# Kernel optimization log

Measured on AMD Instinct MI355X. Metric: run time of the kernel, lower is better.

## Reference

```python
import jax, jax.numpy as jnp
import numpy as np

B, FP, SP = 256, 80, 160          # graphs, features/graph, sentences/graph
H, NH = 128, 4                    # hidden size, attention heads
DH = H // NH
NPG = FP + SP + 2                 # nodes per graph (features, sents, user, item)
N = B * NPG                       # total nodes = 61952
E = 1_000_000


def setup_inputs() -> dict:
    key = jax.random.key(0)
    ks = jax.random.split(key, 24)
    s = 0.05  # small init like the module's uniform(-0.001,0.001) spirit, but non-degenerate
    inp = {
        "fid": jax.random.randint(ks[0], (B * FP,), 0, 10000, dtype=jnp.int32),
        "sid": jax.random.randint(ks[1], (B * SP,), 0, 500000, dtype=jnp.int32),
        "uid": jax.random.randint(ks[2], (B,), 0, 100000, dtype=jnp.int32),
        "iid": jax.random.randint(ks[3], (B,), 0, 50000, dtype=jnp.int32),
        "edge_src": jax.random.randint(ks[4], (E,), 0, N, dtype=jnp.int32),
        "edge_dst": jax.random.randint(ks[5], (E,), 0, N, dtype=jnp.int32),
        "user_tab": jax.random.normal(ks[6], (100000, H), jnp.float32),
        "item_tab": jax.random.normal(ks[7], (50000, H), jnp.float32),
        "feat_tab": jax.random.normal(ks[8], (10000, H), jnp.float32),
        "sent_tab": jax.random.normal(ks[9], (500000, H), jnp.float32),
        "W_feat": jax.random.normal(ks[10], (H, H), jnp.float32) * s,
        "W_sent": jax.random.normal(ks[11], (H, H), jnp.float32) * s,
        "W_user": jax.random.normal(ks[12], (H, H), jnp.float32) * s,
        "W_item": jax.random.normal(ks[13], (H, H), jnp.float32) * s,
        "W_gat": jax.random.normal(ks[14], (H, H), jnp.float32) * s,
        "attn_l": jax.random.normal(ks[15], (NH, DH), jnp.float32) * s,
        "attn_r": jax.random.normal(ks[16], (NH, DH), jnp.float32) * s,
        "w_sent_out": jax.random.normal(ks[17], (H, 1), jnp.float32) * s,
        "b_sent_out": jnp.zeros((1,), jnp.float32),
        "w_feat_out": jax.random.normal(ks[18], (H, 1), jnp.float32) * s,
        "b_feat_out": jnp.zeros((1,), jnp.float32),
    }
    return inp


def _forward(fid, sid, uid, iid, edge_src, edge_dst,
             user_tab, item_tab, feat_tab, sent_tab,
             W_feat, W_sent, W_user, W_item,
             W_gat, attn_l, attn_r,
             w_sent_out, b_sent_out, w_feat_out, b_feat_out):
    # --- embed + bias-free projection for each node type ---
    f_node = feat_tab[fid] @ W_feat          # [B*FP, H]
    s_node = sent_tab[sid] @ W_sent          # [B*SP, H]
    u_node = user_tab[uid] @ W_user          # [B, H]
    i_node = item_tab[iid] @ W_item          # [B, H]

    # --- per-graph node layout: [features | sentences | user | item] ---
    x = jnp.concatenate([
        f_node.reshape(B, FP, H),
        s_node.reshape(B, SP, H),
        u_node[:, None, :],
        i_node[:, None, :],
    ], axis=1).reshape(N, H)                 # [N, H]

    # --- single-layer multi-head GAT over edge list ---
    z = (x @ W_gat).reshape(N, NH, DH)       # [N, NH, DH]
    el = jnp.sum(z * attn_l, axis=-1)        # [N, NH]
    er = jnp.sum(z * attn_r, axis=-1)        # [N, NH]
    e = jax.nn.leaky_relu(el[edge_src] + er[edge_dst], 0.2)  # [E, NH]
    m = jax.ops.segment_max(e, edge_dst, num_segments=N)     # per-dst max
    ex = jnp.exp(e - m[edge_dst])
    den = jax.ops.segment_sum(ex, edge_dst, num_segments=N)
    alpha = ex / (den[edge_dst] + 1e-9)                      # edge softmax [E, NH]
    agg = jax.ops.segment_sum(alpha[:, :, None] * z[edge_src], edge_dst,
                              num_segments=N)                # [N, NH, DH]
    h = jax.nn.elu(agg.reshape(N, H))                        # [N, H]

    # --- gather sentence / feature node states and score ---
    base = jnp.arange(B)[:, None] * NPG
    f_idx = (base + jnp.arange(FP)[None, :]).reshape(-1)      # [B*FP]
    s_idx = (base + FP + jnp.arange(SP)[None, :]).reshape(-1)  # [B*SP]
    sent_scores = (h[s_idx] @ w_sent_out + b_sent_out)[:, 0]  # [B*SP]
    feat_scores = (h[f_idx] @ w_feat_out + b_feat_out)[:, 0]  # [B*FP]
    return jnp.concatenate([sent_scores, feat_scores])        # [B*(SP+FP)]


def reference(fid, sid, uid, iid, edge_src, edge_dst,
              user_tab, item_tab, feat_tab, sent_tab,
              W_feat, W_sent, W_user, W_item,
              W_gat, attn_l, attn_r,
              w_sent_out, b_sent_out, w_feat_out, b_feat_out):
    return _forward(fid, sid, uid, iid, edge_src, edge_dst,
                    user_tab, item_tab, feat_tab, sent_tab,
                    W_feat, W_sent, W_user, W_item,
                    W_gat, attn_l, attn_r,
                    w_sent_out, b_sent_out, w_feat_out, b_feat_out)
```

## Files before the change

kernel.cpp:

```cpp
#include <hip/hip_runtime.h>
#include <cmath>

#define BB  256
#define FPN 80
#define SPN 160
#define NPGc 242
#define NNc (BB*NPGc)
#define NBKT 242
#define CAPSH 13
#define BCAP (1<<CAPSH)
#define NPART 512

typedef __attribute__((ext_vector_type(8))) short bf16x8;
typedef __attribute__((ext_vector_type(4))) float f32x4;

static __device__ __forceinline__ unsigned short f2bf(float f) {
    unsigned u = __float_as_uint(f);
    unsigned r = (u + 0x7fffu + ((u >> 16) & 1u)) >> 16;
    return (unsigned short)r;
}
static __device__ __forceinline__ float bf2f(unsigned short u) {
    return __uint_as_float(((unsigned)u) << 16);
}
static __device__ __forceinline__ unsigned pk2(float a, float b) {
    return (unsigned)f2bf(a) | ((unsigned)f2bf(b) << 16);
}

__global__ __launch_bounds__(256) void k_wc(
    const float* __restrict__ Wf, const float* __restrict__ Ws,
    const float* __restrict__ Wu, const float* __restrict__ Wi,
    const float* __restrict__ Wg, unsigned short* __restrict__ WcT,
    int* __restrict__ bucket_cur)
{
    int b = blockIdx.x;
    int t = threadIdx.x;
    if (b >= 64) {
        if (t < NBKT) bucket_cur[t * 16] = t << CAPSH;
        return;
    }
    int type = b >> 4;
    int rowbase = (b & 15) * 8;
    const float* Wt = type == 0 ? Wf : type == 1 ? Ws : type == 2 ? Wu : Wi;
    int j = t & 127;
    int half = t >> 7;
    for (int i = rowbase + half; i < rowbase + 8; i += 2) {
        float acc = 0.f;
        for (int k = 0; k < 128; ++k)
            acc = fmaf(Wt[i * 128 + k], Wg[k * 128 + j], acc);
        WcT[type * 16384 + j * 128 + i] = f2bf(acc);
    }
}

__global__ __launch_bounds__(256) void k_part(
    const int* __restrict__ esrc, const int* __restrict__ edst, int E,
    int* __restrict__ bucket_cur, unsigned* __restrict__ bucketed)
{
    __shared__ int h[NBKT];
    __shared__ int base_[NBKT];
    int b = blockIdx.x, t = threadIdx.x;
    for (int j = t; j < NBKT; j += 256) h[j] = 0;
    __syncthreads();
    int CH = (E + NPART - 1) / NPART;
    int start = b * CH, lim = min(start + CH, E);
    for (int i = start + t; i < lim; i += 256)
        atomicAdd(&h[edst[i] >> 8], 1);
    __syncthreads();
    for (int j = t; j < NBKT; j += 256) {
        int c = h[j];
        base_[j] = c ? atomicAdd(&bucket_cur[j * 16], c) : 0;
        h[j] = 0;
    }
    __syncthreads();
    for (int i = start + t; i < lim; i += 256) {
        int d = edst[i];
        int bk = d >> 8;
        int pos = base_[bk] + atomicAdd(&h[bk], 1);
        bucketed[pos] = ((unsigned)(d & 255) << 16) | (unsigned)esrc[i];
    }
}

struct SortSh { int h[256]; unsigned short s16[BCAP]; };
struct EmbSh  { unsigned short sWt[128 * 128], sE[32 * 128], sZ[32 * 128]; };
union  ShU    { SortSh sort; EmbSh emb; };

__global__ __launch_bounds__(256) void k_fused(
    const int* __restrict__ bucket_cur, const unsigned* __restrict__ bucketed,
    unsigned short* __restrict__ srcs16, int* __restrict__ off, int* __restrict__ cnt,
    const int* __restrict__ fid, const int* __restrict__ sid,
    const int* __restrict__ uid, const int* __restrict__ iid,
    const float* __restrict__ feat_tab, const float* __restrict__ sent_tab,
    const float* __restrict__ user_tab, const float* __restrict__ item_tab,
    const unsigned short* __restrict__ WcT, const float* __restrict__ attn_l,
    const float* __restrict__ attn_r,
    unsigned short* __restrict__ zb, float* __restrict__ el, float* __restrict__ er)
{
    __shared__ ShU sh;
    int b = blockIdx.x, t = threadIdx.x;

    if (b < NBKT) {
        int bk = b;
        int beg = bk << CAPSH;
        int m = bucket_cur[bk * 16] - beg;
        int* h = sh.sort.h;
        h[t] = 0;
        __syncthreads();
        for (int i = t; i < m; i += 256)
            atomicAdd(&h[(bucketed[beg + i] >> 16) & 255], 1);
        __syncthreads();
        int myc = h[t];
        for (int d = 1; d < 256; d <<= 1) {
            int add = (t >= d) ? h[t - d] : 0;
            __syncthreads();
            h[t] += add;
            __syncthreads();
        }
        int node = (bk << 8) + t;
        off[node] = beg + h[t] - myc;
        cnt[node] = myc;
        __syncthreads();
        for (int i = t; i < m; i += 256) {
            unsigned u = bucketed[beg + i];
            int low = (u >> 16) & 255;
            int pos = atomicSub(&h[low], 1) - 1;
            sh.sort.s16[pos] = (unsigned short)(u & 0xFFFFu);
        }
        __syncthreads();
        for (int i = t; i < m; i += 256) srcs16[beg + i] = sh.sort.s16[i];
        return;
    }

    int eb = b - NBKT;
    int type, q0;
    if (eb < 640)       { type = 0; q0 = eb * 32; }
    else if (eb < 1920) { type = 1; q0 = (eb - 640) * 32; }
    else if (eb < 1928) { type = 2; q0 = (eb - 1920) * 32; }
    else                { type = 3; q0 = (eb - 1928) * 32; }

    {
        const uint4* src = (const uint4*)(WcT + type * 16384);
        uint4* dst = (uint4*)sh.emb.sWt;
#pragma unroll
        for (int i = 0; i < 8; ++i) dst[t + i * 256] = src[t + i * 256];
    }

    int row = t >> 3, part = t & 7;
    int q = q0 + row;
    int id; const float* tab;
    if (type == 0)      { id = fid[q]; tab = feat_tab; }
    else if (type == 1) { id = sid[q]; tab = sent_tab; }
    else if (type == 2) { id = uid[q]; tab = user_tab; }
    else                { id = iid[q]; tab = item_tab; }
    {
        const float4* gsrc = (const float4*)(tab + (long long)id * 128) + part * 4;
        float4 v0 = gsrc[0], v1 = gsrc[1], v2 = gsrc[2], v3 = gsrc[3];
        uint4 p0 = {pk2(v0.x, v0.y), pk2(v0.z, v0.w), pk2(v1.x, v1.y), pk2(v1.z, v1.w)};
        uint4 p1 = {pk2(v2.x, v2.y), pk2(v2.z, v2.w), pk2(v3.x, v3.y), pk2(v3.z, v3.w)};
        uint4* se = (uint4*)&sh.emb.sE[row * 128 + part * 16];
        se[0] = p0; se[1] = p1;
    }
    __syncthreads();

    {
        int lane = t & 63, w = t >> 6;
        int l15 = lane & 15, l4 = lane >> 4;
        int cb = w * 32;
        f32x4 acc00 = {0, 0, 0, 0}, acc01 = {0, 0, 0, 0};
        f32x4 acc10 = {0, 0, 0, 0}, acc11 = {0, 0, 0, 0};
        const unsigned short* sE = sh.emb.sE;
        const unsigned short* sWt = sh.emb.sWt;
#pragma unroll
        for (int kb = 0; kb < 4; ++kb) {
            int ko = kb * 32 + l4 * 8;
            bf16x8 a0 = *(const bf16x8*)&sE[l15 * 128 + ko];
            bf16x8 a1 = *(const bf16x8*)&sE[(l15 + 16) * 128 + ko];
            bf16x8 b0 = *(const bf16x8*)&sWt[(cb + l15) * 128 + ko];
            bf16x8 b1 = *(const bf16x8*)&sWt[(cb + 16 + l15) * 128 + ko];
            acc00 = __builtin_amdgcn_mfma_f32_16x16x32_bf16(a0, b0, acc00, 0, 0, 0);
            acc01 = __builtin_amdgcn_mfma_f32_16x16x32_bf16(a0, b1, acc01, 0, 0, 0);
            acc10 = __builtin_amdgcn_mfma_f32_16x16x32_bf16(a1, b0, acc10, 0, 0, 0);
            acc11 = __builtin_amdgcn_mfma_f32_16x16x32_bf16(a1, b1, acc11, 0, 0, 0);
        }
        unsigned short* sZ = sh.emb.sZ;
#pragma unroll
        for (int reg = 0; reg < 4; ++reg) {
            int r0 = l4 * 4 + reg;
            sZ[r0 * 128 + cb + l15]              = f2bf(acc00[reg]);
            sZ[r0 * 128 + cb + 16 + l15]         = f2bf(acc01[reg]);
            sZ[(r0 + 16) * 128 + cb + l15]       = f2bf(acc10[reg]);
            sZ[(r0 + 16) * 128 + cb + 16 + l15]  = f2bf(acc11[reg]);
        }
    }
    __syncthreads();

    auto nodeof = [&](int qq) -> int {
        if (type == 0) return (qq / 80) * NPGc + (qq % 80);
        if (type == 1) return (qq / 160) * NPGc + 80 + (qq % 160);
        if (type == 2) return qq * NPGc + 240;
        return qq * NPGc + 241;
    };

    {
        int nd = nodeof(q0 + row);
        uint4* zdst = (uint4*)(zb + (size_t)nd * 128 + part * 16);
        const uint4* zsrc = (const uint4*)&sh.emb.sZ[row * 128 + part * 16];
        zdst[0] = zsrc[0]; zdst[1] = zsrc[1];
    }

    if (t < 128) {
        int r = t >> 2, hh = t & 3;
        const unsigned short* zr = &sh.emb.sZ[r * 128 + hh * 32];
        const float* al = attn_l + hh * 32;
        const float* ar_ = attn_r + hh * 32;
        float sl = 0.f, sr = 0.f;
#pragma unroll
        for (int j2 = 0; j2 < 32; ++j2) {
            float zv = bf2f(zr[j2]);
            sl = fmaf(zv, al[j2], sl);
            sr = fmaf(zv, ar_[j2], sr);
        }
        int nd = nodeof(q0 + r);
        el[nd * 4 + hh] = sl;
        er[nd * 4 + hh] = sr;
    }
}

__global__ __launch_bounds__(256) void k_agg(const int* __restrict__ off,
    const int* __restrict__ cnt,
    const unsigned short* __restrict__ src16, const float* __restrict__ el,
    const float* __restrict__ er, const unsigned short* __restrict__ zb,
    const float* __restrict__ w_sent, const float* __restrict__ b_sent,
    const float* __restrict__ w_feat, const float* __restrict__ b_feat,
    float* __restrict__ out)
{
    int lane = threadIdx.x & 63;
    int n = blockIdx.x * 4 + (threadIdx.x >> 6);
    int local = n % NPGc;
    if (local >= FPN + SPN) return;
    int g = n / NPGc;
    int beg = off[n], end = beg + cnt[n];
    float4 er4 = *(const float4*)(er + n * 4);

    int h2 = lane >> 5;
    int li = lane & 31;
    int hm = li >> 3;

    float4 den = {0, 0, 0, 0};
    float4 acc = {0, 0, 0, 0};

    for (int base = beg; base < end; base += 64) {
        int m = min(64, end - base);
        float4 ex = {0, 0, 0, 0};
        int s = 0;
        if (lane < m) {
            s = (int)src16[base + lane];
            float4 l4 = *(const float4*)(el + s * 4);
            float4 e;
            e.x = l4.x + er4.x; e.y = l4.y + er4.y; e.z = l4.z + er4.z; e.w = l4.w + er4.w;
            e.x = e.x > 0.f ? e.x : 0.2f * e.x;
            e.y = e.y > 0.f ? e.y : 0.2f * e.y;
            e.z = e.z > 0.f ? e.z : 0.2f * e.z;
            e.w = e.w > 0.f ? e.w : 0.2f * e.w;
            ex.x = expf(e.x); ex.y = expf(e.y);
            ex.z = expf(e.z); ex.w = expf(e.w);
            den.x += ex.x; den.y += ex.y; den.z += ex.z; den.w += ex.w;
        }
        for (int c0 = 0; c0 < m; c0 += 8) {
            int ss[4]; float ew[4];
#pragma unroll
            for (int k = 0; k < 4; ++k) {
                int c = c0 + 2 * k + h2;
                int cc = c < m ? c : 0;
                ss[k] = __shfl(s, cc);
                float e0 = __shfl(ex.x, cc), e1 = __shfl(ex.y, cc);
                float e2 = __shfl(ex.z, cc), e3 = __shfl(ex.w, cc);
                float eh = hm == 0 ? e0 : hm == 1 ? e1 : hm == 2 ? e2 : e3;
                ew[k] = c < m ? eh : 0.f;
            }
            ushort4 u[4];
#pragma unroll
            for (int k = 0; k < 4; ++k)
                u[k] = *(const ushort4*)(zb + (size_t)ss[k] * 128 + li * 4);
#pragma unroll
            for (int k = 0; k < 4; ++k) {
                acc.x = fmaf(ew[k], bf2f(u[k].x), acc.x);
                acc.y = fmaf(ew[k], bf2f(u[k].y), acc.y);
                acc.z = fmaf(ew[k], bf2f(u[k].z), acc.z);
                acc.w = fmaf(ew[k], bf2f(u[k].w), acc.w);
            }
        }
    }

    acc.x += __shfl_xor(acc.x, 32);
    acc.y += __shfl_xor(acc.y, 32);
    acc.z += __shfl_xor(acc.z, 32);
    acc.w += __shfl_xor(acc.w, 32);
#pragma unroll
    for (int d = 1; d < 64; d <<= 1) {
        den.x += __shfl_xor(den.x, d); den.y += __shfl_xor(den.y, d);
        den.z += __shfl_xor(den.z, d); den.w += __shfl_xor(den.w, d);
    }

    float dh = (hm == 0 ? den.x : hm == 1 ? den.y : hm == 2 ? den.z : den.w) + 1e-9f;
    float vx = acc.x / dh, vy = acc.y / dh, vz = acc.z / dh, vw = acc.w / dh;
    vx = vx > 0.f ? vx : expm1f(vx);
    vy = vy > 0.f ? vy : expm1f(vy);
    vz = vz > 0.f ? vz : expm1f(vz);
    vw = vw > 0.f ? vw : expm1f(vw);

    const float* w; float bias; int oidx;
    if (local < FPN) { w = w_feat; bias = b_feat[0]; oidx = BB * SPN + g * FPN + local; }
    else             { w = w_sent; bias = b_sent[0]; oidx = g * SPN + (local - FPN); }

    float4 w4 = *(const float4*)(w + li * 4);
    float p = vx * w4.x + vy * w4.y + vz * w4.z + vw * w4.w;
#pragma unroll
    for (int d = 1; d < 32; d <<= 1) p += __shfl_xor(p, d);
    if (lane == 0) out[oidx] = p + bias;
}

extern "C" void kernel_launch(void* const* d_in, const int* in_sizes, int n_in,
                              void* d_out, int out_size, void* d_ws, size_t ws_size,
                              hipStream_t stream)
{
    const int* fid = (const int*)d_in[0];
    const int* sid = (const int*)d_in[1];
    const int* uid = (const int*)d_in[2];
    const int* iid = (const int*)d_in[3];
    const int* esrc = (const int*)d_in[4];
    const int* edst = (const int*)d_in[5];
    const float* user_tab = (const float*)d_in[6];
    const float* item_tab = (const float*)d_in[7];
    const float* feat_tab = (const float*)d_in[8];
    const float* sent_tab = (const float*)d_in[9];
    const float* W_feat = (const float*)d_in[10];
    const float* W_sent = (const float*)d_in[11];
    const float* W_user = (const float*)d_in[12];
    const float* W_item = (const float*)d_in[13];
    const float* W_gat  = (const float*)d_in[14];
    const float* attn_l = (const float*)d_in[15];
    const float* attn_r = (const float*)d_in[16];
    const float* w_sent = (const float*)d_in[17];
    const float* b_sent = (const float*)d_in[18];
    const float* w_feat = (const float*)d_in[19];
    const float* b_feat = (const float*)d_in[20];
    int E = in_sizes[4];
    float* out = (float*)d_out;

    char* p = (char*)d_ws;
    auto alloc = [&](size_t bytes) { char* r = p; p += ((bytes + 255) & ~(size_t)255); return r; };
    unsigned short* WcT   = (unsigned short*)alloc((size_t)4 * 128 * 128 * sizeof(unsigned short));
    unsigned short* zb    = (unsigned short*)alloc((size_t)NNc * 128 * sizeof(unsigned short));
    float*          el    = (float*)alloc((size_t)NNc * 4 * sizeof(float));
    float*          er    = (float*)alloc((size_t)NNc * 4 * sizeof(float));
    int*            cnt   = (int*)alloc((size_t)NNc * sizeof(int));
    int*            off   = (int*)alloc((size_t)NNc * sizeof(int));
    int*            bcur  = (int*)alloc((size_t)NBKT * 16 * sizeof(int));
    unsigned*       bktd  = (unsigned*)alloc((size_t)NBKT * BCAP * sizeof(unsigned));
    unsigned short* srcs16= (unsigned short*)alloc((size_t)NBKT * BCAP * sizeof(unsigned short));

    hipLaunchKernelGGL(k_wc, dim3(65), dim3(256), 0, stream,
                       W_feat, W_sent, W_user, W_item, W_gat, WcT, bcur);
    hipLaunchKernelGGL(k_part, dim3(NPART), dim3(256), 0, stream, esrc, edst, E, bcur, bktd);
    hipLaunchKernelGGL(k_fused, dim3(NBKT + 1936), dim3(256), 0, stream,
                       bcur, bktd, srcs16, off, cnt,
                       fid, sid, uid, iid, feat_tab, sent_tab, user_tab, item_tab,
                       WcT, attn_l, attn_r, zb, el, er);
    hipLaunchKernelGGL(k_agg, dim3(NNc / 4), dim3(256), 0, stream,
                       off, cnt, srcs16, el, er, zb, w_sent, b_sent, w_feat, b_feat, out);
}
```

Before: 123.5 us.

## Merge weight-combine into partition kernel and widen aggregation gathers via LDS staging

The weight-combine blocks now run as extra blocks of the edge-partition kernel, and the bucket counters are zeroed with a memset. The cursor offset is folded into the partition base, so one launch is dropped. The aggregation kernel stages source ids and exp weights in LDS instead of shuffling them. Each 16-lane group now gathers a full 256-byte bf16 row with 16-byte loads, four edges at a time. The grid also launches only output nodes (240 per graph) rather than all nodes with early exit. The trade-off is extra LDS traffic and a cross-group reduction, in exchange for wider memory transactions and fewer idle waves.

```diff
diff --git a/kernel.cpp b/kernel.cpp
--- a/kernel.cpp
+++ b/kernel.cpp
@@ -22,42 +22,37 @@
 static __device__ __forceinline__ float bf2f(unsigned short u) {
     return __uint_as_float(((unsigned)u) << 16);
 }
+static __device__ __forceinline__ float bflo(unsigned u) { return __uint_as_float(u << 16); }
+static __device__ __forceinline__ float bfhi(unsigned u) { return __uint_as_float(u & 0xffff0000u); }
 static __device__ __forceinline__ unsigned pk2(float a, float b) {
     return (unsigned)f2bf(a) | ((unsigned)f2bf(b) << 16);
 }
 
-__global__ __launch_bounds__(256) void k_wc(
+__global__ __launch_bounds__(256) void k_partwc(
+    const int* __restrict__ esrc, const int* __restrict__ edst, int E,
+    int* __restrict__ bucket_cur, unsigned* __restrict__ bucketed,
     const float* __restrict__ Wf, const float* __restrict__ Ws,
     const float* __restrict__ Wu, const float* __restrict__ Wi,
-    const float* __restrict__ Wg, unsigned short* __restrict__ WcT,
-    int* __restrict__ bucket_cur)
+    const float* __restrict__ Wg, unsigned short* __restrict__ WcT)
 {
-    int b = blockIdx.x;
-    int t = threadIdx.x;
-    if (b >= 64) {
-        if (t < NBKT) bucket_cur[t * 16] = t << CAPSH;
+    int b = blockIdx.x, t = threadIdx.x;
+    if (b >= NPART) {
+        int wb = b - NPART;
+        int type = wb >> 4;
+        int rowbase = (wb & 15) * 8;
+        const float* Wt = type == 0 ? Wf : type == 1 ? Ws : type == 2 ? Wu : Wi;
+        int j = t & 127;
+        int half = t >> 7;
+        for (int i = rowbase + half; i < rowbase + 8; i += 2) {
+            float acc = 0.f;
+            for (int k = 0; k < 128; ++k)
+                acc = fmaf(Wt[i * 128 + k], Wg[k * 128 + j], acc);
+            WcT[type * 16384 + j * 128 + i] = f2bf(acc);
+        }
         return;
     }
-    int type = b >> 4;
-    int rowbase = (b & 15) * 8;
-    const float* Wt = type == 0 ? Wf : type == 1 ? Ws : type == 2 ? Wu : Wi;
-    int j = t & 127;
-    int half = t >> 7;
-    for (int i = rowbase + half; i < rowbase + 8; i += 2) {
-        float acc = 0.f;
-        for (int k = 0; k < 128; ++k)
-            acc = fmaf(Wt[i * 128 + k], Wg[k * 128 + j], acc);
-        WcT[type * 16384 + j * 128 + i] = f2bf(acc);
-    }
-}
-
-__global__ __launch_bounds__(256) void k_part(
-    const int* __restrict__ esrc, const int* __restrict__ edst, int E,
-    int* __restrict__ bucket_cur, unsigned* __restrict__ bucketed)
-{
     __shared__ int h[NBKT];
     __shared__ int base_[NBKT];
-    int b = blockIdx.x, t = threadIdx.x;
     for (int j = t; j < NBKT; j += 256) h[j] = 0;
     __syncthreads();
     int CH = (E + NPART - 1) / NPART;
@@ -67,7 +62,7 @@
     __syncthreads();
     for (int j = t; j < NBKT; j += 256) {
         int c = h[j];
-        base_[j] = c ? atomicAdd(&bucket_cur[j * 16], c) : 0;
+        base_[j] = (j << CAPSH) + (c ? atomicAdd(&bucket_cur[j * 16], c) : 0);
         h[j] = 0;
     }
     __syncthreads();
@@ -100,7 +95,7 @@
     if (b < NBKT) {
         int bk = b;
         int beg = bk << CAPSH;
-        int m = bucket_cur[bk * 16] - beg;
+        int m = bucket_cur[bk * 16];
         int* h = sh.sort.h;
         h[t] = 0;
         __syncthreads();
@@ -232,27 +227,26 @@
     const float* __restrict__ w_feat, const float* __restrict__ b_feat,
     float* __restrict__ out)
 {
-    int lane = threadIdx.x & 63;
-    int n = blockIdx.x * 4 + (threadIdx.x >> 6);
-    int local = n % NPGc;
-    if (local >= FPN + SPN) return;
-    int g = n / NPGc;
-    int beg = off[n], end = beg + cnt[n];
-    float4 er4 = *(const float4*)(er + n * 4);
-
-    int h2 = lane >> 5;
-    int li = lane & 31;
-    int hm = li >> 3;
+    __shared__ int   ssrc[4][64];
+    __shared__ float sex[4][64][4];
+    int t = threadIdx.x;
+    int w = t >> 6, lane = t & 63;
+    int oid = blockIdx.x * 4 + w;
+    int g = oid / 240, local = oid % 240;
+    int n = g * NPGc + local;
+    int beg = off[n], deg = cnt[n];
+    const float4 er4 = *(const float4*)(er + n * 4);
+
+    int grp = lane >> 4, li = lane & 15;
+    int hm = li >> 2;
 
     float4 den = {0, 0, 0, 0};
-    float4 acc = {0, 0, 0, 0};
-
-    for (int base = beg; base < end; base += 64) {
-        int m = min(64, end - base);
-        float4 ex = {0, 0, 0, 0};
-        int s = 0;
+    float acc[8] = {0, 0, 0, 0, 0, 0, 0, 0};
+
+    for (int chunk = 0; chunk < deg; chunk += 64) {
+        int m = min(64, deg - chunk);
         if (lane < m) {
-            s = (int)src16[base + lane];
+            int s = (int)src16[beg + chunk + lane];
             float4 l4 = *(const float4*)(el + s * 4);
             float4 e;
             e.x = l4.x + er4.x; e.y = l4.y + er4.y; e.z = l4.z + er4.z; e.w = l4.w + er4.w;
@@ -260,40 +254,33 @@
             e.y = e.y > 0.f ? e.y : 0.2f * e.y;
             e.z = e.z > 0.f ? e.z : 0.2f * e.z;
             e.w = e.w > 0.f ? e.w : 0.2f * e.w;
-            ex.x = expf(e.x); ex.y = expf(e.y);
-            ex.z = expf(e.z); ex.w = expf(e.w);
+            float4 ex;
+            ex.x = expf(e.x); ex.y = expf(e.y); ex.z = expf(e.z); ex.w = expf(e.w);
             den.x += ex.x; den.y += ex.y; den.z += ex.z; den.w += ex.w;
-        }
-        for (int c0 = 0; c0 < m; c0 += 8) {
-            int ss[4]; float ew[4];
-#pragma unroll
-            for (int k = 0; k < 4; ++k) {
-                int c = c0 + 2 * k + h2;
-                int cc = c < m ? c : 0;
-                ss[k] = __shfl(s, cc);
-                float e0 = __shfl(ex.x, cc), e1 = __shfl(ex.y, cc);
-                float e2 = __shfl(ex.z, cc), e3 = __shfl(ex.w, cc);
-                float eh = hm == 0 ? e0 : hm == 1 ? e1 : hm == 2 ? e2 : e3;
-                ew[k] = c < m ? eh : 0.f;
-            }
-            ushort4 u[4];
-#pragma unroll
-            for (int k = 0; k < 4; ++k)
-                u[k] = *(const ushort4*)(zb + (size_t)ss[k] * 128 + li * 4);
-#pragma unroll
-            for (int k = 0; k < 4; ++k) {
-                acc.x = fmaf(ew[k], bf2f(u[k].x), acc.x);
-                acc.y = fmaf(ew[k], bf2f(u[k].y), acc.y);
-                acc.z = fmaf(ew[k], bf2f(u[k].z), acc.z);
-                acc.w = fmaf(ew[k], bf2f(u[k].w), acc.w);
-            }
-        }
-    }
-
-    acc.x += __shfl_xor(acc.x, 32);
-    acc.y += __shfl_xor(acc.y, 32);
-    acc.z += __shfl_xor(acc.z, 32);
-    acc.w += __shfl_xor(acc.w, 32);
+            ssrc[w][lane] = s;
+            *(float4*)&sex[w][lane][0] = ex;
+        }
+        for (int c0 = 0; c0 < m; c0 += 4) {
+            int j = c0 + grp;
+            float ew = 0.f; int s = 0;
+            if (j < m) { s = ssrc[w][j]; ew = sex[w][j][hm]; }
+            uint4 u = *(const uint4*)(zb + (size_t)s * 128 + li * 8);
+            acc[0] = fmaf(ew, bflo(u.x), acc[0]);
+            acc[1] = fmaf(ew, bfhi(u.x), acc[1]);
+            acc[2] = fmaf(ew, bflo(u.y), acc[2]);
+            acc[3] = fmaf(ew, bfhi(u.y), acc[3]);
+            acc[4] = fmaf(ew, bflo(u.z), acc[4]);
+            acc[5] = fmaf(ew, bfhi(u.z), acc[5]);
+            acc[6] = fmaf(ew, bflo(u.w), acc[6]);
+            acc[7] = fmaf(ew, bfhi(u.w), acc[7]);
+        }
+    }
+
+#pragma unroll
+    for (int k = 0; k < 8; ++k) {
+        acc[k] += __shfl_xor(acc[k], 16);
+        acc[k] += __shfl_xor(acc[k], 32);
+    }
 #pragma unroll
     for (int d = 1; d < 64; d <<= 1) {
         den.x += __shfl_xor(den.x, d); den.y += __shfl_xor(den.y, d);
@@ -301,20 +288,23 @@
     }
 
     float dh = (hm == 0 ? den.x : hm == 1 ? den.y : hm == 2 ? den.z : den.w) + 1e-9f;
-    float vx = acc.x / dh, vy = acc.y / dh, vz = acc.z / dh, vw = acc.w / dh;
-    vx = vx > 0.f ? vx : expm1f(vx);
-    vy = vy > 0.f ? vy : expm1f(vy);
-    vz = vz > 0.f ? vz : expm1f(vz);
-    vw = vw > 0.f ? vw : expm1f(vw);
-
-    const float* w; float bias; int oidx;
-    if (local < FPN) { w = w_feat; bias = b_feat[0]; oidx = BB * SPN + g * FPN + local; }
-    else             { w = w_sent; bias = b_sent[0]; oidx = g * SPN + (local - FPN); }
-
-    float4 w4 = *(const float4*)(w + li * 4);
-    float p = vx * w4.x + vy * w4.y + vz * w4.z + vw * w4.w;
-#pragma unroll
-    for (int d = 1; d < 32; d <<= 1) p += __shfl_xor(p, d);
+    float hv[8];
+#pragma unroll
+    for (int k = 0; k < 8; ++k) {
+        float v = acc[k] / dh;
+        hv[k] = v > 0.f ? v : expm1f(v);
+    }
+
+    const float* wv; float bias; int oidx;
+    if (local < FPN) { wv = w_feat; bias = b_feat[0]; oidx = BB * SPN + g * FPN + local; }
+    else             { wv = w_sent; bias = b_sent[0]; oidx = g * SPN + (local - FPN); }
+
+    float4 wa = *(const float4*)(wv + li * 8);
+    float4 wb = *(const float4*)(wv + li * 8 + 4);
+    float p = hv[0] * wa.x + hv[1] * wa.y + hv[2] * wa.z + hv[3] * wa.w
+            + hv[4] * wb.x + hv[5] * wb.y + hv[6] * wb.z + hv[7] * wb.w;
+#pragma unroll
+    for (int d = 1; d < 16; d <<= 1) p += __shfl_xor(p, d);
     if (lane == 0) out[oidx] = p + bias;
 }
 
@@ -358,13 +348,14 @@
     unsigned*       bktd  = (unsigned*)alloc((size_t)NBKT * BCAP * sizeof(unsigned));
     unsigned short* srcs16= (unsigned short*)alloc((size_t)NBKT * BCAP * sizeof(unsigned short));
 
-    hipLaunchKernelGGL(k_wc, dim3(65), dim3(256), 0, stream,
-                       W_feat, W_sent, W_user, W_item, W_gat, WcT, bcur);
-    hipLaunchKernelGGL(k_part, dim3(NPART), dim3(256), 0, stream, esrc, edst, E, bcur, bktd);
+    hipMemsetAsync(bcur, 0, (size_t)NBKT * 16 * sizeof(int), stream);
+    hipLaunchKernelGGL(k_partwc, dim3(NPART + 64), dim3(256), 0, stream,
+                       esrc, edst, E, bcur, bktd,
+                       W_feat, W_sent, W_user, W_item, W_gat, WcT);
     hipLaunchKernelGGL(k_fused, dim3(NBKT + 1936), dim3(256), 0, stream,
                        bcur, bktd, srcs16, off, cnt,
                        fid, sid, uid, iid, feat_tab, sent_tab, user_tab, item_tab,
                        WcT, attn_l, attn_r, zb, el, er);
-    hipLaunchKernelGGL(k_agg, dim3(NNc / 4), dim3(256), 0, stream,
+    hipLaunchKernelGGL(k_agg, dim3(BB * 240 / 4), dim3(256), 0, stream,
                        off, cnt, srcs16, el, er, zb, w_sent, b_sent, w_feat, b_feat, out);
 }
```

Result: no change. 123.3 us (-0.2%).
